# Kernel optimization log

Measured on AMD Instinct MI355X. Metric: run time of the kernel, lower is better.

Reference implementation:

```python
import jax, jax.numpy as jnp
import numpy as np

B, T, I, H, O = 256, 512, 128, 256, 1


def setup_inputs() -> dict:
    key = jax.random.key(0)
    ks = jax.random.split(key, 7)
    s_ih = 1.0 / np.sqrt(H)
    return {
        "x": jax.random.normal(ks[0], (B, T, I), dtype=jnp.float32),
        "W_ih": jax.random.uniform(ks[1], (H, I), jnp.float32, -s_ih, s_ih),
        "W_hh": jax.random.uniform(ks[2], (H, H), jnp.float32, -s_ih, s_ih),
        "b_ih": jax.random.uniform(ks[3], (H,), jnp.float32, -s_ih, s_ih),
        "b_hh": jax.random.uniform(ks[4], (H,), jnp.float32, -s_ih, s_ih),
        "fc_w": jax.random.uniform(ks[5], (O, H), jnp.float32, -s_ih, s_ih),
        "fc_b": jax.random.uniform(ks[6], (O,), jnp.float32, -s_ih, s_ih),
    }


def reference(x, W_ih, W_hh, b_ih, b_hh, fc_w, fc_b):
    # Elman RNN (tanh), batch_first, single layer, h0 = zeros.
    # Only the last hidden state feeds the fc head, so scan carries h only.
    b = b_ih + b_hh
    xW = jnp.einsum('bti,hi->tbh', x, W_ih) + b  # precompute input projection [T,B,H]

    def step(h, xw_t):
        h = jnp.tanh(xw_t + h @ W_hh.T)
        return h, None

    h0 = jnp.zeros((x.shape[0], W_hh.shape[0]), dtype=x.dtype)
    h_last, _ = jax.lax.scan(step, h0, xW)
    return h_last @ fc_w.T + fc_b  # [B, O]
```

## Files before the change

kernel.cpp:

```cpp
#include <hip/hip_runtime.h>
#include <hip/hip_bf16.h>

#define B_ 256
#define T_ 512
#define I_ 128
#define H_ 256

typedef __bf16 bf16x8 __attribute__((ext_vector_type(8)));
typedef float  f32x4  __attribute__((ext_vector_type(4)));
typedef unsigned short u16;
typedef unsigned int   u32;

union U16x8Cast { uint4 v; bf16x8 b; };

__device__ inline u16 f2b(float f) {
    union { __bf16 h; u16 u; } c; c.h = (__bf16)f; return c.u;
}
__device__ inline bf16x8 pack8(float4 lo, float4 hi) {
    bf16x8 f;
    f[0]=(__bf16)lo.x; f[1]=(__bf16)lo.y; f[2]=(__bf16)lo.z; f[3]=(__bf16)lo.w;
    f[4]=(__bf16)hi.x; f[5]=(__bf16)hi.y; f[6]=(__bf16)hi.z; f[7]=(__bf16)hi.w;
    return f;
}
__device__ inline uint2 pack4(float a, float b, float c, float d) {
    uint2 p;
    p.x = (u32)f2b(a) | ((u32)f2b(b) << 16);
    p.y = (u32)f2b(c) | ((u32)f2b(d) << 16);
    return p;
}
__device__ inline f32x4 b4_to_f32x4(uint2 u) {
    f32x4 r;
    r[0] = __uint_as_float(u.x << 16);
    r[1] = __uint_as_float(u.x & 0xFFFF0000u);
    r[2] = __uint_as_float(u.y << 16);
    r[3] = __uint_as_float(u.y & 0xFFFF0000u);
    return r;
}
__device__ inline float fast_tanh(float x) {
    float e = __expf(2.f * x);
    float d = 1.f + e;
    float r;
    asm("v_rcp_f32 %0, %1" : "=v"(r) : "v"(d));
    return fmaf(-2.f, r, 1.f);
}

#define WG_BARRIER() asm volatile("s_waitcnt lgkmcnt(0)\n\ts_barrier" ::: "memory")

#define LDST 264
__global__ __launch_bounds__(256, 2) void xw_gemm_mfma(const float* __restrict__ x,
                                                       const float* __restrict__ W_ih,
                                                       const float* __restrict__ b_ih,
                                                       const float* __restrict__ b_hh,
                                                       u16* __restrict__ xw) {
    __shared__ u16 tile[64 * LDST];

    const int tid  = (int)threadIdx.x;
    const int wave = tid >> 6;
    const int lane = tid & 63;
    const int q    = lane >> 4;
    const int ml   = lane & 15;
    const int m0   = (int)blockIdx.x * 128;
    const int b    = m0 >> 9;
    const int t0   = m0 & 511;
    const int n0   = wave * 64;

    bf16x8 wA[4][4];
#pragma unroll
    for (int tau = 0; tau < 4; ++tau) {
        const float* wr = W_ih + (size_t)(n0 + tau * 16 + ml) * I_;
#pragma unroll
        for (int kap = 0; kap < 4; ++kap) {
            const int k0 = kap * 32 + q * 8;
            wA[tau][kap] = pack8(*(const float4*)(wr + k0), *(const float4*)(wr + k0 + 4));
        }
    }

    f32x4 acc[8][4];
#pragma unroll
    for (int mt = 0; mt < 8; ++mt)
#pragma unroll
        for (int tau = 0; tau < 4; ++tau) acc[mt][tau] = (f32x4)0.f;

#pragma unroll
    for (int kap = 0; kap < 4; ++kap) {
        bf16x8 xB[8];
#pragma unroll
        for (int mt = 0; mt < 8; ++mt) {
            const float* xr = x + (size_t)(m0 + mt * 16 + ml) * I_ + kap * 32 + q * 8;
            xB[mt] = pack8(*(const float4*)xr, *(const float4*)(xr + 4));
        }
#pragma unroll
        for (int mt = 0; mt < 8; ++mt)
#pragma unroll
            for (int tau = 0; tau < 4; ++tau)
                acc[mt][tau] = __builtin_amdgcn_mfma_f32_16x16x32_bf16(
                    wA[tau][kap], xB[mt], acc[mt][tau], 0, 0, 0);
    }

    float4 bias4[4];
#pragma unroll
    for (int tau = 0; tau < 4; ++tau) {
        const int n = n0 + tau * 16 + q * 4;
        float4 bi = *(const float4*)(b_ih + n);
        float4 bh = *(const float4*)(b_hh + n);
        bias4[tau] = make_float4(bi.x + bh.x, bi.y + bh.y, bi.z + bh.z, bi.w + bh.w);
    }

#pragma unroll
    for (int p = 0; p < 2; ++p) {
        if (p) __syncthreads();
#pragma unroll
        for (int mt = 0; mt < 4; ++mt) {
            const int row = mt * 16 + ml;
            const int mg  = p * 4 + mt;
#pragma unroll
            for (int tau = 0; tau < 4; ++tau) {
                uint2 pk = pack4(acc[mg][tau][0] + bias4[tau].x,
                                 acc[mg][tau][1] + bias4[tau].y,
                                 acc[mg][tau][2] + bias4[tau].z,
                                 acc[mg][tau][3] + bias4[tau].w);
                *(uint2*)(tile + row * LDST + n0 + tau * 16 + q * 4) = pk;
            }
        }
        __syncthreads();
#pragma unroll
        for (int s = 0; s < 4; ++s) {
            const int rr = s * 16 + (tid >> 4);
            const int c  = tid & 15;
            const uint4* srcp = (const uint4*)(tile + rr * LDST);
            uint4* dstp = (uint4*)(xw + ((size_t)(t0 + p * 64 + rr) * B_ + b) * H_);
            uint4 v0 = srcp[c];
            uint4 v1 = srcp[c + 16];
            dstp[c] = v0;
            dstp[c + 16] = v1;
        }
    }
}

__global__ __launch_bounds__(512, 2) void rnn_scan_mfma(const u16* __restrict__ xw,
                                                        const float* __restrict__ W_hh,
                                                        const float* __restrict__ fc_w,
                                                        const float* __restrict__ fc_b,
                                                        float* __restrict__ out) {
    __shared__ __attribute__((aligned(16))) u16 hbuf[2][4096];
    __shared__ float red[8][16];

    const int tid  = (int)threadIdx.x;
    const int wave = tid >> 6;
    const int lane = tid & 63;
    const int q    = lane >> 4;
    const int m    = lane & 15;
    const int b0   = (int)blockIdx.x * 16;

    bf16x8 wf[2][8];
#pragma unroll
    for (int tau2 = 0; tau2 < 2; ++tau2) {
        const float* wr = W_hh + (size_t)(wave * 32 + tau2 * 16 + m) * H_;
#pragma unroll
        for (int kap = 0; kap < 8; ++kap) {
            const int k0 = kap * 32 + q * 8;
            wf[tau2][kap] = pack8(*(const float4*)(wr + k0), *(const float4*)(wr + k0 + 4));
        }
    }

    int widx[2];
#pragma unroll
    for (int tau2 = 0; tau2 < 2; ++tau2) {
        const int nbw = wave * 32 + tau2 * 16 + q * 4;
        widx[tau2] = (nbw >> 5) * 512 + (((nbw >> 3) & 3) * 16 + m) * 8 + (nbw & 7);
    }

    {
        uint4* p = (uint4*)&hbuf[0][0];
        const uint4 z = {0u, 0u, 0u, 0u};
        p[tid] = z;
    }
    WG_BARRIER();

    const u16* xwp = xw + (size_t)(b0 + m) * H_ + (wave * 32 + q * 4);
    const size_t tstride = (size_t)B_ * H_;

    uint2 pfA[2], pfB[2];
    pfA[0] = *(const uint2*)(xwp);
    pfA[1] = *(const uint2*)(xwp + 16);
    pfB[0] = *(const uint2*)(xwp + tstride);
    pfB[1] = *(const uint2*)(xwp + tstride + 16);

    int cur = 0;
    f32x4 acc[2];
    for (int tt = 0; tt < T_ / 2; ++tt) {
        {
            const int t = 2 * tt;
            acc[0] = b4_to_f32x4(pfA[0]);
            acc[1] = b4_to_f32x4(pfA[1]);
            if (t + 2 < T_) {
                const u16* pt = xwp + (size_t)(t + 2) * tstride;
                pfA[0] = *(const uint2*)(pt);
                pfA[1] = *(const uint2*)(pt + 16);
            }
            const uint4* hb = (const uint4*)&hbuf[cur][0];
#pragma unroll
            for (int kap = 0; kap < 8; ++kap) {
                U16x8Cast c; c.v = hb[kap * 64 + lane];
                acc[0] = __builtin_amdgcn_mfma_f32_16x16x32_bf16(wf[0][kap], c.b, acc[0], 0, 0, 0);
                acc[1] = __builtin_amdgcn_mfma_f32_16x16x32_bf16(wf[1][kap], c.b, acc[1], 0, 0, 0);
            }
            u16* wb = &hbuf[cur ^ 1][0];
#pragma unroll
            for (int tau2 = 0; tau2 < 2; ++tau2) {
                uint2 pk = pack4(fast_tanh(acc[tau2][0]), fast_tanh(acc[tau2][1]),
                                 fast_tanh(acc[tau2][2]), fast_tanh(acc[tau2][3]));
                *(uint2*)(wb + widx[tau2]) = pk;
            }
            WG_BARRIER();
            cur ^= 1;
        }
        {
            const int t = 2 * tt + 1;
            acc[0] = b4_to_f32x4(pfB[0]);
            acc[1] = b4_to_f32x4(pfB[1]);
            if (t + 2 < T_) {
                const u16* pt = xwp + (size_t)(t + 2) * tstride;
                pfB[0] = *(const uint2*)(pt);
                pfB[1] = *(const uint2*)(pt + 16);
            }
            const uint4* hb = (const uint4*)&hbuf[cur][0];
#pragma unroll
            for (int kap = 0; kap < 8; ++kap) {
                U16x8Cast c; c.v = hb[kap * 64 + lane];
                acc[0] = __builtin_amdgcn_mfma_f32_16x16x32_bf16(wf[0][kap], c.b, acc[0], 0, 0, 0);
                acc[1] = __builtin_amdgcn_mfma_f32_16x16x32_bf16(wf[1][kap], c.b, acc[1], 0, 0, 0);
            }
            if (t != T_ - 1) {
                u16* wb = &hbuf[cur ^ 1][0];
#pragma unroll
                for (int tau2 = 0; tau2 < 2; ++tau2) {
                    uint2 pk = pack4(fast_tanh(acc[tau2][0]), fast_tanh(acc[tau2][1]),
                                     fast_tanh(acc[tau2][2]), fast_tanh(acc[tau2][3]));
                    *(uint2*)(wb + widx[tau2]) = pk;
                }
                WG_BARRIER();
                cur ^= 1;
            }
        }
    }

    float4 fcw[2];
#pragma unroll
    for (int tau2 = 0; tau2 < 2; ++tau2)
        fcw[tau2] = *(const float4*)(fc_w + wave * 32 + tau2 * 16 + q * 4);

    float partial = 0.f;
#pragma unroll
    for (int tau2 = 0; tau2 < 2; ++tau2) {
        partial += fast_tanh(acc[tau2][0]) * fcw[tau2].x;
        partial += fast_tanh(acc[tau2][1]) * fcw[tau2].y;
        partial += fast_tanh(acc[tau2][2]) * fcw[tau2].z;
        partial += fast_tanh(acc[tau2][3]) * fcw[tau2].w;
    }
    partial += __shfl_xor(partial, 16);
    partial += __shfl_xor(partial, 32);
    __syncthreads();
    if (lane < 16) red[wave][m] = partial;
    __syncthreads();
    if (tid < 16) {
        float s = red[0][tid] + red[1][tid] + red[2][tid] + red[3][tid]
                + red[4][tid] + red[5][tid] + red[6][tid] + red[7][tid];
        out[b0 + tid] = s + fc_b[0];
    }
}

extern "C" void kernel_launch(void* const* d_in, const int* in_sizes, int n_in,
                              void* d_out, int out_size, void* d_ws, size_t ws_size,
                              hipStream_t stream) {
    const float* x    = (const float*)d_in[0];
    const float* W_ih = (const float*)d_in[1];
    const float* W_hh = (const float*)d_in[2];
    const float* b_ih = (const float*)d_in[3];
    const float* b_hh = (const float*)d_in[4];
    const float* fc_w = (const float*)d_in[5];
    const float* fc_b = (const float*)d_in[6];
    float* out = (float*)d_out;

    u16* xwbuf = (u16*)d_ws;
    xw_gemm_mfma<<<(B_ * T_) / 128, 256, 0, stream>>>(x, W_ih, b_ih, b_hh, xwbuf);
    rnn_scan_mfma<<<B_ / 16, 512, 0, stream>>>(xwbuf, W_hh, fc_w, fc_b, out);
}
```

Baseline: 371.1 us.

## Halve scan waves per block and fold tanh scaling into weights

The recurrent scan kernel now runs 4 waves of 256 threads instead of 8, and each wave computes 64 hidden units with four MFMA accumulators. This halves the number of waves joining each per-step barrier and gives each wave more independent MFMA work. Both weight matrices and the bias are pre-scaled by 2/ln2, so tanh can use the raw v_exp_f32 (base-2 exponent) and skip a multiply. The cost is more registers per wave for the extra weight fragments and slightly different rounding from scaling before the bf16 conversion.

New measurement: 452.5 us. 1.22x slower.

```diff
diff --git a/kernel.cpp b/kernel.cpp
--- a/kernel.cpp
+++ b/kernel.cpp
@@ -6,6 +6,8 @@
 #define I_ 128
 #define H_ 256
 
+#define SC 2.885390081777927f
+
 typedef __bf16 bf16x8 __attribute__((ext_vector_type(8)));
 typedef float  f32x4  __attribute__((ext_vector_type(4)));
 typedef unsigned short u16;
@@ -16,10 +18,10 @@
 __device__ inline u16 f2b(float f) {
     union { __bf16 h; u16 u; } c; c.h = (__bf16)f; return c.u;
 }
-__device__ inline bf16x8 pack8(float4 lo, float4 hi) {
+__device__ inline bf16x8 pack8s(float4 lo, float4 hi, float s) {
     bf16x8 f;
-    f[0]=(__bf16)lo.x; f[1]=(__bf16)lo.y; f[2]=(__bf16)lo.z; f[3]=(__bf16)lo.w;
-    f[4]=(__bf16)hi.x; f[5]=(__bf16)hi.y; f[6]=(__bf16)hi.z; f[7]=(__bf16)hi.w;
+    f[0]=(__bf16)(lo.x*s); f[1]=(__bf16)(lo.y*s); f[2]=(__bf16)(lo.z*s); f[3]=(__bf16)(lo.w*s);
+    f[4]=(__bf16)(hi.x*s); f[5]=(__bf16)(hi.y*s); f[6]=(__bf16)(hi.z*s); f[7]=(__bf16)(hi.w*s);
     return f;
 }
 __device__ inline uint2 pack4(float a, float b, float c, float d) {
@@ -36,8 +38,9 @@
     r[3] = __uint_as_float(u.y & 0xFFFF0000u);
     return r;
 }
-__device__ inline float fast_tanh(float x) {
-    float e = __expf(2.f * x);
+__device__ inline float tanh_pre(float s) {
+    float e;
+    asm("v_exp_f32 %0, %1" : "=v"(e) : "v"(s));
     float d = 1.f + e;
     float r;
     asm("v_rcp_f32 %0, %1" : "=v"(r) : "v"(d));
@@ -71,7 +74,7 @@
 #pragma unroll
         for (int kap = 0; kap < 4; ++kap) {
             const int k0 = kap * 32 + q * 8;
-            wA[tau][kap] = pack8(*(const float4*)(wr + k0), *(const float4*)(wr + k0 + 4));
+            wA[tau][kap] = pack8s(*(const float4*)(wr + k0), *(const float4*)(wr + k0 + 4), SC);
         }
     }
 
@@ -87,7 +90,7 @@
 #pragma unroll
         for (int mt = 0; mt < 8; ++mt) {
             const float* xr = x + (size_t)(m0 + mt * 16 + ml) * I_ + kap * 32 + q * 8;
-            xB[mt] = pack8(*(const float4*)xr, *(const float4*)(xr + 4));
+            xB[mt] = pack8s(*(const float4*)xr, *(const float4*)(xr + 4), 1.f);
         }
 #pragma unroll
         for (int mt = 0; mt < 8; ++mt)
@@ -103,7 +106,8 @@
         const int n = n0 + tau * 16 + q * 4;
         float4 bi = *(const float4*)(b_ih + n);
         float4 bh = *(const float4*)(b_hh + n);
-        bias4[tau] = make_float4(bi.x + bh.x, bi.y + bh.y, bi.z + bh.z, bi.w + bh.w);
+        bias4[tau] = make_float4((bi.x + bh.x) * SC, (bi.y + bh.y) * SC,
+                                 (bi.z + bh.z) * SC, (bi.w + bh.w) * SC);
     }
 
 #pragma unroll
@@ -137,13 +141,13 @@
     }
 }
 
-__global__ __launch_bounds__(512, 2) void rnn_scan_mfma(const u16* __restrict__ xw,
+__global__ __launch_bounds__(256, 1) void rnn_scan_mfma(const u16* __restrict__ xw,
                                                         const float* __restrict__ W_hh,
                                                         const float* __restrict__ fc_w,
                                                         const float* __restrict__ fc_b,
                                                         float* __restrict__ out) {
     __shared__ __attribute__((aligned(16))) u16 hbuf[2][4096];
-    __shared__ float red[8][16];
+    __shared__ float red[4][16];
 
     const int tid  = (int)threadIdx.x;
     const int wave = tid >> 6;
@@ -152,92 +156,95 @@
     const int m    = lane & 15;
     const int b0   = (int)blockIdx.x * 16;
 
-    bf16x8 wf[2][8];
-#pragma unroll
-    for (int tau2 = 0; tau2 < 2; ++tau2) {
-        const float* wr = W_hh + (size_t)(wave * 32 + tau2 * 16 + m) * H_;
+    bf16x8 wf[4][8];
+#pragma unroll
+    for (int tau = 0; tau < 4; ++tau) {
+        const float* wr = W_hh + (size_t)(wave * 64 + tau * 16 + m) * H_;
 #pragma unroll
         for (int kap = 0; kap < 8; ++kap) {
             const int k0 = kap * 32 + q * 8;
-            wf[tau2][kap] = pack8(*(const float4*)(wr + k0), *(const float4*)(wr + k0 + 4));
-        }
-    }
-
-    int widx[2];
-#pragma unroll
-    for (int tau2 = 0; tau2 < 2; ++tau2) {
-        const int nbw = wave * 32 + tau2 * 16 + q * 4;
-        widx[tau2] = (nbw >> 5) * 512 + (((nbw >> 3) & 3) * 16 + m) * 8 + (nbw & 7);
+            wf[tau][kap] = pack8s(*(const float4*)(wr + k0), *(const float4*)(wr + k0 + 4), SC);
+        }
+    }
+
+    int widx[4];
+#pragma unroll
+    for (int tau = 0; tau < 4; ++tau) {
+        const int nbw = wave * 64 + tau * 16 + q * 4;
+        widx[tau] = (nbw >> 5) * 512 + (((nbw >> 3) & 3) * 16 + m) * 8 + (nbw & 7);
     }
 
     {
         uint4* p = (uint4*)&hbuf[0][0];
         const uint4 z = {0u, 0u, 0u, 0u};
         p[tid] = z;
+        p[tid + 256] = z;
     }
     WG_BARRIER();
 
-    const u16* xwp = xw + (size_t)(b0 + m) * H_ + (wave * 32 + q * 4);
+    const u16* xwp = xw + (size_t)(b0 + m) * H_ + (wave * 64 + q * 4);
     const size_t tstride = (size_t)B_ * H_;
 
-    uint2 pfA[2], pfB[2];
-    pfA[0] = *(const uint2*)(xwp);
-    pfA[1] = *(const uint2*)(xwp + 16);
-    pfB[0] = *(const uint2*)(xwp + tstride);
-    pfB[1] = *(const uint2*)(xwp + tstride + 16);
+    uint2 pfA[4], pfB[4];
+#pragma unroll
+    for (int tau = 0; tau < 4; ++tau) pfA[tau] = *(const uint2*)(xwp + tau * 16);
+#pragma unroll
+    for (int tau = 0; tau < 4; ++tau) pfB[tau] = *(const uint2*)(xwp + tstride + tau * 16);
 
     int cur = 0;
-    f32x4 acc[2];
+    f32x4 acc[4];
     for (int tt = 0; tt < T_ / 2; ++tt) {
         {
             const int t = 2 * tt;
-            acc[0] = b4_to_f32x4(pfA[0]);
-            acc[1] = b4_to_f32x4(pfA[1]);
+#pragma unroll
+            for (int tau = 0; tau < 4; ++tau) acc[tau] = b4_to_f32x4(pfA[tau]);
             if (t + 2 < T_) {
                 const u16* pt = xwp + (size_t)(t + 2) * tstride;
-                pfA[0] = *(const uint2*)(pt);
-                pfA[1] = *(const uint2*)(pt + 16);
+#pragma unroll
+                for (int tau = 0; tau < 4; ++tau) pfA[tau] = *(const uint2*)(pt + tau * 16);
             }
             const uint4* hb = (const uint4*)&hbuf[cur][0];
 #pragma unroll
             for (int kap = 0; kap < 8; ++kap) {
                 U16x8Cast c; c.v = hb[kap * 64 + lane];
-                acc[0] = __builtin_amdgcn_mfma_f32_16x16x32_bf16(wf[0][kap], c.b, acc[0], 0, 0, 0);
-                acc[1] = __builtin_amdgcn_mfma_f32_16x16x32_bf16(wf[1][kap], c.b, acc[1], 0, 0, 0);
+#pragma unroll
+                for (int tau = 0; tau < 4; ++tau)
+                    acc[tau] = __builtin_amdgcn_mfma_f32_16x16x32_bf16(wf[tau][kap], c.b, acc[tau], 0, 0, 0);
             }
             u16* wb = &hbuf[cur ^ 1][0];
 #pragma unroll
-            for (int tau2 = 0; tau2 < 2; ++tau2) {
-                uint2 pk = pack4(fast_tanh(acc[tau2][0]), fast_tanh(acc[tau2][1]),
-                                 fast_tanh(acc[tau2][2]), fast_tanh(acc[tau2][3]));
-                *(uint2*)(wb + widx[tau2]) = pk;
+            for (int tau = 0; tau < 4; ++tau) {
+                uint2 pk = pack4(tanh_pre(acc[tau][0]), tanh_pre(acc[tau][1]),
+                                 tanh_pre(acc[tau][2]), tanh_pre(acc[tau][3]));
+                *(uint2*)(wb + widx[tau]) = pk;
             }
             WG_BARRIER();
             cur ^= 1;
         }
         {
             const int t = 2 * tt + 1;
-            acc[0] = b4_to_f32x4(pfB[0]);
-            acc[1] = b4_to_f32x4(pfB[1]);
+#pragma unroll
+            for (int tau = 0; tau < 4; ++tau) acc[tau] = b4_to_f32x4(pfB[tau]);
             if (t + 2 < T_) {
                 const u16* pt = xwp + (size_t)(t + 2) * tstride;
-                pfB[0] = *(const uint2*)(pt);
-                pfB[1] = *(const uint2*)(pt + 16);
+#pragma unroll
+                for (int tau = 0; tau < 4; ++tau) pfB[tau] = *(const uint2*)(pt + tau * 16);
             }
             const uint4* hb = (const uint4*)&hbuf[cur][0];
 #pragma unroll
             for (int kap = 0; kap < 8; ++kap) {
                 U16x8Cast c; c.v = hb[kap * 64 + lane];
-                acc[0] = __builtin_amdgcn_mfma_f32_16x16x32_bf16(wf[0][kap], c.b, acc[0], 0, 0, 0);
-                acc[1] = __builtin_amdgcn_mfma_f32_16x16x32_bf16(wf[1][kap], c.b, acc[1], 0, 0, 0);
+#pragma unroll
+                for (int tau = 0; tau < 4; ++tau)
+                    acc[tau] = __builtin_amdgcn_mfma_f32_16x16x32_bf16(wf[tau][kap], c.b, acc[tau], 0, 0, 0);
             }
             if (t != T_ - 1) {
                 u16* wb = &hbuf[cur ^ 1][0];
 #pragma unroll
-                for (int tau2 = 0; tau2 < 2; ++tau2) {
-                    uint2 pk = pack4(fast_tanh(acc[tau2][0]), fast_tanh(acc[tau2][1]),
-                                     fast_tanh(acc[tau2][2]), fast_tanh(acc[tau2][3]));
-                    *(uint2*)(wb + widx[tau2]) = pk;
+                for (int tau = 0; tau < 4; ++tau) {
+                    uint2 pk = pack4(tanh_pre(acc[tau][0]), tanh_pre(acc[tau][1]),
+                                     tanh_pre(acc[tau][2]), tanh_pre(acc[tau][3]));
+                    *(uint2*)(wb + widx[tau]) = pk;
                 }
                 WG_BARRIER();
                 cur ^= 1;
@@ -245,27 +252,25 @@
         }
     }
 
-    float4 fcw[2];
-#pragma unroll
-    for (int tau2 = 0; tau2 < 2; ++tau2)
-        fcw[tau2] = *(const float4*)(fc_w + wave * 32 + tau2 * 16 + q * 4);
+    float4 fcw[4];
+#pragma unroll
+    for (int tau = 0; tau < 4; ++tau)
+        fcw[tau] = *(const float4*)(fc_w + wave * 64 + tau * 16 + q * 4);
 
     float partial = 0.f;
 #pragma unroll
-    for (int tau2 = 0; tau2 < 2; ++tau2) {
-        partial += fast_tanh(acc[tau2][0]) * fcw[tau2].x;
-        partial += fast_tanh(acc[tau2][1]) * fcw[tau2].y;
-        partial += fast_tanh(acc[tau2][2]) * fcw[tau2].z;
-        partial += fast_tanh(acc[tau2][3]) * fcw[tau2].w;
+    for (int tau = 0; tau < 4; ++tau) {
+        partial += tanh_pre(acc[tau][0]) * fcw[tau].x;
+        partial += tanh_pre(acc[tau][1]) * fcw[tau].y;
+        partial += tanh_pre(acc[tau][2]) * fcw[tau].z;
+        partial += tanh_pre(acc[tau][3]) * fcw[tau].w;
     }
     partial += __shfl_xor(partial, 16);
     partial += __shfl_xor(partial, 32);
-    __syncthreads();
     if (lane < 16) red[wave][m] = partial;
     __syncthreads();
     if (tid < 16) {
-        float s = red[0][tid] + red[1][tid] + red[2][tid] + red[3][tid]
-                + red[4][tid] + red[5][tid] + red[6][tid] + red[7][tid];
+        float s = red[0][tid] + red[1][tid] + red[2][tid] + red[3][tid];
         out[b0 + tid] = s + fc_b[0];
     }
 }
@@ -284,5 +289,5 @@
 
     u16* xwbuf = (u16*)d_ws;
     xw_gemm_mfma<<<(B_ * T_) / 128, 256, 0, stream>>>(x, W_ih, b_ih, b_hh, xwbuf);
-    rnn_scan_mfma<<<B_ / 16, 512, 0, stream>>>(xwbuf, W_hh, fc_w, fc_b, out);
-}
+    rnn_scan_mfma<<<B_ / 16, 256, 0, stream>>>(xwbuf, W_hh, fc_w, fc_b, out);
+}
```
